# Kernel tuning notes

Measured on AMD Instinct MI355X. Metric: run time of the kernel, lower is better.

## Reference

```python
import jax, jax.numpy as jnp
import numpy as np
from jax import lax

H = 64        # hidden_dim
M = 5         # num_modes
T_OUT = 6

def _gru_step(h, x, W_ih, W_hh, b_ih, b_hh):
    # torch GRU/GRUCell math; W_* are [3H, in] torch layout
    gi = x @ W_ih.T + b_ih
    gh = h @ W_hh.T + b_hh
    i_r, i_z, i_n = jnp.split(gi, 3, axis=-1)
    h_r, h_z, h_n = jnp.split(gh, 3, axis=-1)
    r = jax.nn.sigmoid(i_r + h_r)
    z = jax.nn.sigmoid(i_z + h_z)
    n = jnp.tanh(i_n + r * h_n)
    return (1.0 - z) * n + z * h

def _edges(B, N):
    # all ordered pairs i != j per sample (row-major like the python double loop),
    # then self loops for every node (PyG GATConv add_self_loops=True)
    s, d = np.nonzero(~np.eye(N, dtype=bool))
    off = (np.arange(B) * N)[:, None]
    src = (s[None, :] + off).ravel()
    dst = (d[None, :] + off).ravel()
    loops = np.arange(B * N)
    return np.concatenate([src, loops]), np.concatenate([dst, loops]), src.shape[0]

def reference(x, embed_W, embed_b, gat_W, gat_att_src, gat_att_dst, gat_b,
              enc_Wih, enc_Whh, enc_bih, enc_bhh,
              dec_Wih, dec_Whh, dec_bih, dec_bhh,
              out_W1, out_b1, out_W2, out_b2, proj_W, proj_b,
              conf_W1, conf_b1, conf_W2, conf_b2):
    B, T, N, _ = x.shape
    BN = B * N
    x_emb = x @ embed_W + embed_b                      # (B,T,N,H)

    # --- GRU encoder over time, batched over B*N nodes ---
    seq = x_emb.transpose(1, 0, 2, 3).reshape(T, BN, H)
    def enc_step(h, xt):
        return _gru_step(h, xt, enc_Wih, enc_Whh, enc_bih, enc_bhh), None
    h_enc, _ = lax.scan(enc_step, jnp.zeros((BN, H), x.dtype), seq)  # (BN,H)

    # --- GATConv (1 head, eval mode => no dropout) on last-frame embeddings ---
    mask = (x[:, -1, :, 0:6].sum(-1) != 0).reshape(BN)
    src_np, dst_np, n_pair = _edges(B, N)
    src = jnp.asarray(src_np); dst = jnp.asarray(dst_np)
    valid = jnp.concatenate([mask[src[:n_pair]] & mask[dst[:n_pair]],
                             jnp.ones((BN,), bool)])  # self loops always present
    xl = x_emb[:, -1].reshape(BN, H) @ gat_W           # (BN,H) transformed feats
    a_s = xl @ gat_att_src                             # (BN,)
    a_d = xl @ gat_att_dst
    alpha = jax.nn.leaky_relu(a_s[src] + a_d[dst], 0.2)
    amax = jax.ops.segment_max(jnp.where(valid, alpha, -1e30), dst, num_segments=BN)
    e = jnp.where(valid, jnp.exp(alpha - amax[dst]), 0.0)
    denom = jax.ops.segment_sum(e, dst, num_segments=BN)
    w = e / denom[dst]
    gat_out = jax.ops.segment_sum(w[:, None] * xl[src], dst, num_segments=BN) + gat_b

    h_final = h_enc + gat_out                          # (BN,H)

    # --- GRUCell decoder loop ---
    dec_in = (x[:, -1, :, 0:2] @ proj_W + proj_b).reshape(BN, H)
    def dec_step(carry, _):
        h, di = carry
        h = _gru_step(h, di, dec_Wih, dec_Whh, dec_bih, dec_bhh)
        o = jax.nn.relu(h @ out_W1 + out_b1) @ out_W2 + out_b2   # (BN, 2M)
        o = o.reshape(B, N, 2, M)
        nxt = (o[..., 0] @ proj_W + proj_b).reshape(BN, H)       # mode-0 xy fed back
        return (h, nxt), o
    _, outs = lax.scan(dec_step, (h_final, dec_in), None, length=T_OUT)  # (T_OUT,B,N,2,M)
    traj = outs.transpose(1, 4, 2, 0, 3)               # (B, M, N, T_OUT, 2)

    hf = h_final.reshape(B, N, H)
    conf = jax.nn.softmax(jax.nn.relu(hf @ conf_W1 + conf_b1) @ conf_W2 + conf_b2, axis=-1)
    return traj, conf.transpose(0, 2, 1)               # (B, M, N)

def setup_inputs() -> dict:
    key = jax.random.key(0)
    ks = jax.random.split(key, 25)
    n = lambda k, s: jax.random.normal(k, s, jnp.float32) * 0.1
    B, T, N, Fd = 32768, 5, 5, 10
    return {
        "x": jax.random.normal(ks[0], (B, T, N, Fd), jnp.float32),
        "embed_W": n(ks[1], (Fd, H)), "embed_b": n(ks[2], (H,)),
        "gat_W": n(ks[3], (H, H)), "gat_att_src": n(ks[4], (H,)),
        "gat_att_dst": n(ks[5], (H,)), "gat_b": n(ks[6], (H,)),
        "enc_Wih": n(ks[7], (3 * H, H)), "enc_Whh": n(ks[8], (3 * H, H)),
        "enc_bih": n(ks[9], (3 * H,)), "enc_bhh": n(ks[10], (3 * H,)),
        "dec_Wih": n(ks[11], (3 * H, H)), "dec_Whh": n(ks[12], (3 * H, H)),
        "dec_bih": n(ks[13], (3 * H,)), "dec_bhh": n(ks[14], (3 * H,)),
        "out_W1": n(ks[15], (H, 64)), "out_b1": n(ks[16], (64,)),
        "out_W2": n(ks[17], (64, 2 * M)), "out_b2": n(ks[18], (2 * M,)),
        "proj_W": n(ks[19], (2, H)), "proj_b": n(ks[20], (H,)),
        "conf_W1": n(ks[21], (H, 64)), "conf_b1": n(ks[22], (64,)),
        "conf_W2": n(ks[23], (64, M)), "conf_b2": n(ks[24], (M,)),
    }
```

## Files before the change

### kernel.cpp

```cpp
#include <hip/hip_runtime.h>

#define HDIM 64
#define NMODE 5
#define TOUT 6
#define TIN 5
#define NNODE 5
#define FD 10

typedef short bf16x8 __attribute__((ext_vector_type(8)));
typedef float f32x4 __attribute__((ext_vector_type(4)));

#define MFMA16(A,B,C) __builtin_amdgcn_mfma_f32_16x16x32_bf16((A),(B),(C),0,0,0)


__device__ __forceinline__ float fastrcp(float x){ return __builtin_amdgcn_rcpf(x); }
__device__ __forceinline__ float sigm(float x){ return fastrcp(1.f + __expf(-x)); }
__device__ __forceinline__ float tanh_f(float x){ return 2.f*fastrcp(1.f + __expf(-2.f*x)) - 1.f; }

__device__ __forceinline__ short f2b(float f){
  unsigned u = __float_as_uint(f);
  unsigned r = (u + 0x7FFFu + ((u >> 16) & 1u)) >> 16;
  return (short)r;
}
__device__ __forceinline__ float b2f(short s){
  return __uint_as_float(((unsigned)(unsigned short)s) << 16);
}
__device__ __forceinline__ int hswz(int row, int col){
  return row*64 + ((((col>>3) ^ (row&7)))<<3) + (col&7);
}

__global__ void setup_kernel(
    const float* __restrict__ embed_W, const float* __restrict__ embed_b,
    const float* __restrict__ enc_Wih, const float* __restrict__ enc_bih,
    const float* __restrict__ enc_Whh, const float* __restrict__ enc_bhh,
    const float* __restrict__ dec_Wih, const float* __restrict__ dec_bih,
    const float* __restrict__ dec_Whh, const float* __restrict__ dec_bhh,
    const float* __restrict__ proj_W,  const float* __restrict__ proj_b,
    const float* __restrict__ gat_W,   const float* __restrict__ gat_as,
    const float* __restrict__ gat_ad,  const float* __restrict__ gat_b,
    const float* __restrict__ out_W1,  const float* __restrict__ out_W2,
    const float* __restrict__ conf_W1, const float* __restrict__ conf_W2,
    short* __restrict__ wsb)
{
  float* wsf  = (float*)(wsb) + 26880;
  float* WcET = wsf;        float* WcDT = wsf+1920;
  float* bcE  = wsf+2304;   float* bcD  = wsf+2496;
  float* brzE = wsf+2688;   float* brzD = wsf+2816;
  float* EG   = wsf+2944;   float* ebg0 = wsf+3584;
  float* egs  = wsf+3648;   float* egd  = wsf+3658;
  float* c6   = wsf+3668;
  const int t = threadIdx.x;

  for (int i = t; i < 1920; i += 256){ int n=i/10, f=i%10; float s=0.f;
    for(int e=0;e<64;e++) s += embed_W[f*64+e]*enc_Wih[n*64+e]; WcET[i]=s; }
  for (int i = t; i < 384; i += 256){ int n=i/2, c=i%2; float s=0.f;
    for(int e=0;e<64;e++) s += proj_W[c*64+e]*dec_Wih[n*64+e]; WcDT[i]=s; }
  for (int n = t; n < 192; n += 256){
    float s=enc_bih[n]; for(int e=0;e<64;e++) s += embed_b[e]*enc_Wih[n*64+e]; bcE[n]=s;
    float d=dec_bih[n]; for(int e=0;e<64;e++) d += proj_b[e]*dec_Wih[n*64+e]; bcD[n]=d; }
  for (int i = t; i < 640; i += 256){ int f=i/64, n=i%64; float s=0.f;
    for(int e=0;e<64;e++) s += embed_W[f*64+e]*gat_W[e*64+n]; EG[i]=s; }
  for (int n = t; n < 64; n += 256){ float s=0.f;
    for(int e=0;e<64;e++) s += embed_b[e]*gat_W[e*64+n]; ebg0[n]=s; }
  __syncthreads();
  for (int n = t; n < 128; n += 256){ brzE[n]=bcE[n]+enc_bhh[n]; brzD[n]=bcD[n]+dec_bhh[n]; }
  for (int f = t; f < 10; f += 256){ float s=0.f, d=0.f;
    for(int n=0;n<64;n++){ s += EG[f*64+n]*gat_as[n]; d += EG[f*64+n]*gat_ad[n]; }
    egs[f]=s; egd[f]=d; }
  if (t == 0){ float s=0.f, d=0.f;
    for(int n=0;n<64;n++){ s += ebg0[n]*gat_as[n]; d += ebg0[n]*gat_ad[n]; }
    c6[0]=s; c6[1]=d; }
  __syncthreads();

  for (int i = t; i < 18432; i += 256){
    int nt=i/1536, r=i%1536, kt=r>>9, r2=r&511, lane=r2>>3, j=r2&7;
    int k=kt*32+(lane>>4)*8+j, n=nt*16+(lane&15);
    float v=0.f;
    if (k < 64) v = enc_Whh[n*64+k];
    else if (k < 74){ if (n < 128) v = WcET[n*10+(k-64)]; }
    else if (k == 74) v = (n < 128) ? brzE[n] : enc_bhh[n];
    wsb[i]=f2b(v);
  }
  for (int i = t; i < 2048; i += 256){
    int nt=i>>9, r2=i&511, lane=r2>>3, j=r2&7;
    int k=64+(lane>>4)*8+j, n=128+nt*16+(lane&15);
    float v=0.f;
    if (k < 74) v = WcET[n*10+(k-64)];
    else if (k == 74) v = bcE[n];
    wsb[18432+i]=f2b(v);
  }
  for (int i = t; i < 18432; i += 256){
    int nt=i/1536, r=i%1536, kt=r>>9, r2=r&511, lane=r2>>3, j=r2&7;
    int k=kt*32+(lane>>4)*8+j, n=nt*16+(lane&15);
    float v=0.f;
    if (k < 64) v = dec_Whh[n*64+k];
    else if (k < 66){ if (n < 128) v = WcDT[n*2+(k-64)]; }
    else if (k == 66) v = (n < 128) ? brzD[n] : dec_bhh[n];
    wsb[20480+i]=f2b(v);
  }
  for (int i = t; i < 2048; i += 256){
    int nt=i>>9, r2=i&511, lane=r2>>3, j=r2&7;
    int k=64+(lane>>4)*8+j, n=128+nt*16+(lane&15);
    float v=0.f;
    if (k < 66) v = WcDT[n*2+(k-64)];
    else if (k == 66) v = bcD[n];
    wsb[38912+i]=f2b(v);
  }
  for (int i = t; i < 2560; i += 256){
    int nt=i>>9, r2=i&511, lane=r2>>3, j=r2&7;
    int k=64+(lane>>4)*8+j, n=nt*16+(lane&15);
    float v=0.f;
    if (k < 74){ int f=k-64;
      if (n < 64) v = EG[f*64+n]; else if (n == 64) v = egs[f]; else if (n == 65) v = egd[f];
    } else if (k == 74){
      if (n < 64) v = ebg0[n]+gat_b[n]; else if (n == 64) v = c6[0]; else if (n == 65) v = c6[1];
    }
    wsb[40960+i]=f2b(v);
  }
  for (int i = t; i < 4096; i += 256){
    int nt=i>>10, r=i&1023, kt=r>>9, r2=r&511, lane=r2>>3, j=r2&7;
    int k=kt*32+(lane>>4)*8+j, n=nt*16+(lane&15);
    wsb[43520+i]=f2b(out_W1 [k*64+n]);
    wsb[48640+i]=f2b(conf_W1[k*64+n]);
  }
  for (int i = t; i < 1024; i += 256){
    int kt=i>>9, r2=i&511, lane=r2>>3, j=r2&7;
    int k=kt*32+(lane>>4)*8+j, n=lane&15;
    wsb[47616+i]=f2b(n<10 ? out_W2 [k*10+n] : 0.f);
    wsb[52736+i]=f2b(n<5  ? conf_W2[k*5 +n] : 0.f);
  }
}

__device__ __forceinline__ void gru_mfma_step(const short* Bs, short* hS,
    float (&hcd)[4][4], bf16x8 af2, int wid, int lane)
{
  const int g = lane>>4, l15 = lane&15;
  const int arow = wid*16 + l15;
  const int sw = arow & 7;
  bf16x8 af0 = *(const bf16x8*)&hS[arow*64 + (((0+g) ^ sw)<<3)];
  bf16x8 af1 = *(const bf16x8*)&hS[arow*64 + (((4+g) ^ sw)<<3)];
  f32x4 acc[12];
  #pragma unroll
  for (int nt = 0; nt < 12; nt++){
    f32x4 a = {0.f,0.f,0.f,0.f};
    a = MFMA16(af0, *(const bf16x8*)&Bs[(nt*3+0)*512 + lane*8], a);
    a = MFMA16(af1, *(const bf16x8*)&Bs[(nt*3+1)*512 + lane*8], a);
    a = MFMA16(af2, *(const bf16x8*)&Bs[(nt*3+2)*512 + lane*8], a);
    acc[nt] = a;
  }
  f32x4 accx[4];
  #pragma unroll
  for (int nt = 0; nt < 4; nt++){
    f32x4 a = {0.f,0.f,0.f,0.f};
    accx[nt] = MFMA16(af2, *(const bf16x8*)&Bs[18432 + nt*512 + lane*8], a);
  }
  #pragma unroll
  for (int nt = 0; nt < 4; nt++){
    #pragma unroll
    for (int j = 0; j < 4; j++){
      float r  = sigm(acc[nt][j]);
      float z  = sigm(acc[nt+4][j]);
      float ng = tanh_f(accx[nt][j] + r*acc[nt+8][j]);
      float hn = (1.f - z)*ng + z*hcd[nt][j];
      hcd[nt][j] = hn;
      hS[hswz(wid*16 + 4*g + j, nt*16 + l15)] = f2b(hn);
    }
  }
}

__global__ __launch_bounds__(256, 2) void model_kernel(
    const float* __restrict__ x, const short* __restrict__ wsb,
    const float* __restrict__ out_b1, const float* __restrict__ out_b2,
    const float* __restrict__ conf_b1, const float* __restrict__ conf_b2,
    float* __restrict__ traj, float* __restrict__ conf, int B)
{
  __shared__ __align__(16) short Bs[20480];
  __shared__ __align__(16) short hS[4096];
  __shared__ __align__(16) short sS[4096];
  __shared__ float xyS[128];
  __shared__ float asdS[128];
  __shared__ float maskS[64];

  const int tid = threadIdx.x;
  const int wid = tid>>6, lane = tid&63;
  const int g = lane>>4, l15 = lane&15;
  const int BN = B*NNODE;
  const int br0 = blockIdx.x*60;
  const int arow = wid*16 + l15;
  const short ONE = 0x3F80;

  float b1r[4], cb1r[4];
  #pragma unroll
  for (int nt = 0; nt < 4; nt++){ b1r[nt]=out_b1[nt*16+l15]; cb1r[nt]=conf_b1[nt*16+l15]; }
  const float b2r  = out_b2 [l15<10 ? l15 : 0];
  const float cb2r = conf_b2[l15<5  ? l15 : 0];

  int growA = br0 + arow; if (growA > BN-1) growA = BN-1;
  const float* xrow = x + (size_t)(growA/5)*250 + (growA%5)*10;

  for (int i = tid; i < 2560; i += 256) ((int4*)Bs)[i] = ((const int4*)wsb)[i];
  for (int i = tid; i < 4096; i += 256) hS[i] = 0;
  float hcd[4][4];
  #pragma unroll
  for (int a1=0;a1<4;a1++){
    #pragma unroll
    for (int a2=0;a2<4;a2++) hcd[a1][a2]=0.f;
  }
  __syncthreads();

  for (int t = 0; t < TIN; t++){
    bf16x8 af2 = {0,0,0,0,0,0,0,0};
    if (g == 0){
      const float2* p = (const float2*)(xrow + t*50);
      float2 v0=p[0], v1=p[1], v2=p[2], v3=p[3];
      af2[0]=f2b(v0.x); af2[1]=f2b(v0.y); af2[2]=f2b(v1.x); af2[3]=f2b(v1.y);
      af2[4]=f2b(v2.x); af2[5]=f2b(v2.y); af2[6]=f2b(v3.x); af2[7]=f2b(v3.y);
    } else if (g == 1){
      const float2* p = (const float2*)(xrow + t*50 + 8);
      float2 v4=p[0];
      af2[0]=f2b(v4.x); af2[1]=f2b(v4.y); af2[2]=ONE;
    }
    gru_mfma_step(Bs, hS, hcd, af2, wid, lane);
    __syncthreads();
  }

  {
    bf16x8 af2 = {0,0,0,0,0,0,0,0};
    if (g == 0){
      const float2* p = (const float2*)(xrow + 4*50);
      float2 v0=p[0], v1=p[1], v2=p[2], v3=p[3];
      af2[0]=f2b(v0.x); af2[1]=f2b(v0.y); af2[2]=f2b(v1.x); af2[3]=f2b(v1.y);
      af2[4]=f2b(v2.x); af2[5]=f2b(v2.y); af2[6]=f2b(v3.x); af2[7]=f2b(v3.y);
      float msum = v0.x+v0.y+v1.x+v1.y+v2.x+v2.y;
      maskS[arow] = (msum != 0.f) ? 1.f : 0.f;
      xyS[arow*2]   = v0.x;
      xyS[arow*2+1] = v0.y;
    } else if (g == 1){
      const float2* p = (const float2*)(xrow + 4*50 + 8);
      float2 v4=p[0];
      af2[0]=f2b(v4.x); af2[1]=f2b(v4.y); af2[2]=ONE;
    }
    #pragma unroll
    for (int nt = 0; nt < 5; nt++){
      f32x4 a = {0.f,0.f,0.f,0.f};
      a = MFMA16(af2, *(const bf16x8*)(wsb + 40960 + nt*512 + lane*8), a);
      if (nt < 4){
        #pragma unroll
        for (int j = 0; j < 4; j++)
          sS[(wid*16 + 4*g + j)*64 + nt*16 + l15] = f2b(a[j]);
      } else if (l15 < 2){
        #pragma unroll
        for (int j = 0; j < 4; j++)
          asdS[(wid*16 + 4*g + j)*2 + l15] = a[j];
      }
    }
  }
  __syncthreads();
  {
    int dst = tid >> 2, cb = tid & 3;
    if (dst < 60){
      int nd = dst % 5, bas = dst - nd;
      float ad  = asdS[dst*2+1];
      float mkD = maskS[dst];
      float al[5], mx = -1e30f;
      #pragma unroll
      for (int i = 0; i < 5; i++){
        float a = asdS[(bas+i)*2] + ad;
        a = (a > 0.f) ? a : 0.2f*a;
        bool valid = (i == nd) || (maskS[bas+i] != 0.f && mkD != 0.f);
        al[i] = valid ? a : -1e30f;
        mx = fmaxf(mx, al[i]);
      }
      float w5[5], es = 0.f;
      #pragma unroll
      for (int i = 0; i < 5; i++){ float e = (al[i] > -1e29f) ? __expf(al[i]-mx) : 0.f; w5[i]=e; es+=e; }
      float rs = fastrcp(es);
      #pragma unroll
      for (int i = 0; i < 5; i++) w5[i] *= rs;
      for (int cc = 0; cc < 16; cc++){
        int c = cb*16 + cc;
        float agg = 0.f;
        #pragma unroll
        for (int i = 0; i < 5; i++) agg += w5[i]*b2f(sS[(bas+i)*64 + c]);
        int hi = hswz(dst, c);
        hS[hi] = f2b(b2f(hS[hi]) + agg);
      }
    }
  }
  __syncthreads();
  #pragma unroll
  for (int nt = 0; nt < 4; nt++){
    #pragma unroll
    for (int j = 0; j < 4; j++)
      hcd[nt][j] = b2f(hS[hswz(wid*16+4*g+j, nt*16+l15)]);
  }

  {
    const int sw = arow & 7;
    bf16x8 hf0 = *(const bf16x8*)&hS[arow*64 + (((0+g) ^ sw)<<3)];
    bf16x8 hf1 = *(const bf16x8*)&hS[arow*64 + (((4+g) ^ sw)<<3)];
    #pragma unroll
    for (int nt = 0; nt < 4; nt++){
      f32x4 a = {0.f,0.f,0.f,0.f};
      a = MFMA16(hf0, *(const bf16x8*)(wsb + 48640 + (nt*2+0)*512 + lane*8), a);
      a = MFMA16(hf1, *(const bf16x8*)(wsb + 48640 + (nt*2+1)*512 + lane*8), a);
      #pragma unroll
      for (int j = 0; j < 4; j++)
        sS[hswz(wid*16+4*g+j, nt*16+l15)] = f2b(fmaxf(a[j] + cb1r[nt], 0.f));
    }
    __syncthreads();
    bf16x8 sf0 = *(const bf16x8*)&sS[arow*64 + (((0+g) ^ sw)<<3)];
    bf16x8 sf1 = *(const bf16x8*)&sS[arow*64 + (((4+g) ^ sw)<<3)];
    f32x4 a = {0.f,0.f,0.f,0.f};
    a = MFMA16(sf0, *(const bf16x8*)(wsb + 52736 + 0*512 + lane*8), a);
    a = MFMA16(sf1, *(const bf16x8*)(wsb + 52736 + 1*512 + lane*8), a);
    #pragma unroll
    for (int j = 0; j < 4; j++){
      float my = a[j] + cb2r;
      float v0 = __shfl(my, (lane&48)+0, 64);
      float v1 = __shfl(my, (lane&48)+1, 64);
      float v2 = __shfl(my, (lane&48)+2, 64);
      float v3 = __shfl(my, (lane&48)+3, 64);
      float v4 = __shfl(my, (lane&48)+4, 64);
      float mx = fmaxf(fmaxf(fmaxf(v0,v1),fmaxf(v2,v3)),v4);
      float es = __expf(v0-mx)+__expf(v1-mx)+__expf(v2-mx)+__expf(v3-mx)+__expf(v4-mx);
      int lrow = wid*16 + 4*g + j;
      int gr = br0 + lrow;
      if (l15 < 5 && lrow < 60 && gr < BN){
        int samp = gr/5, node = gr - samp*5;
        conf[((size_t)samp*NMODE + l15)*NNODE + node] = __expf(my-mx)*fastrcp(es);
      }
    }
    __syncthreads();
  }

  for (int i = tid; i < 2560; i += 256) ((int4*)Bs)[i] = ((const int4*)(wsb + 20480))[i];
  __syncthreads();

  for (int t = 0; t < TOUT; t++){
    bf16x8 af2 = {0,0,0,0,0,0,0,0};
    if (g == 0){
      af2[0] = f2b(xyS[arow*2]);
      af2[1] = f2b(xyS[arow*2+1]);
      af2[2] = ONE;
    }
    gru_mfma_step(Bs, hS, hcd, af2, wid, lane);
    __syncthreads();

    const int sw = arow & 7;
    bf16x8 hf0 = *(const bf16x8*)&hS[arow*64 + (((0+g) ^ sw)<<3)];
    bf16x8 hf1 = *(const bf16x8*)&hS[arow*64 + (((4+g) ^ sw)<<3)];
    #pragma unroll
    for (int nt = 0; nt < 4; nt++){
      f32x4 a = {0.f,0.f,0.f,0.f};
      a = MFMA16(hf0, *(const bf16x8*)(wsb + 43520 + (nt*2+0)*512 + lane*8), a);
      a = MFMA16(hf1, *(const bf16x8*)(wsb + 43520 + (nt*2+1)*512 + lane*8), a);
      #pragma unroll
      for (int j = 0; j < 4; j++)
        sS[hswz(wid*16+4*g+j, nt*16+l15)] = f2b(fmaxf(a[j] + b1r[nt], 0.f));
    }
    __syncthreads();
    bf16x8 sf0 = *(const bf16x8*)&sS[arow*64 + (((0+g) ^ sw)<<3)];
    bf16x8 sf1 = *(const bf16x8*)&sS[arow*64 + (((4+g) ^ sw)<<3)];
    f32x4 oo = {0.f,0.f,0.f,0.f};
    oo = MFMA16(sf0, *(const bf16x8*)(wsb + 47616 + 0*512 + lane*8), oo);
    oo = MFMA16(sf1, *(const bf16x8*)(wsb + 47616 + 1*512 + lane*8), oo);
    #pragma unroll
    for (int j = 0; j < 4; j++){
      float ov = oo[j] + b2r;
      int lrow = wid*16 + 4*g + j;
      int gr = br0 + lrow;
      if (l15 < 10 && lrow < 60 && gr < BN){
        int samp = gr/5, node = gr - samp*5;
        int cc = (l15 >= 5) ? 1 : 0;
        int m = l15 - 5*cc;
        traj[((size_t)(samp*NMODE + m)*NNODE + node)*(TOUT*2) + t*2 + cc] = ov;
      }
      if (l15 == 0) xyS[lrow*2]   = ov;
      if (l15 == 5) xyS[lrow*2+1] = ov;
    }
    __syncthreads();
  }
}

extern "C" void kernel_launch(void* const* d_in, const int* in_sizes, int n_in,
                              void* d_out, int out_size, void* d_ws, size_t ws_size,
                              hipStream_t stream)
{
  const float* x           = (const float*)d_in[0];
  const float* embed_W     = (const float*)d_in[1];
  const float* embed_b     = (const float*)d_in[2];
  const float* gat_W       = (const float*)d_in[3];
  const float* gat_att_src = (const float*)d_in[4];
  const float* gat_att_dst = (const float*)d_in[5];
  const float* gat_b       = (const float*)d_in[6];
  const float* enc_Wih     = (const float*)d_in[7];
  const float* enc_Whh     = (const float*)d_in[8];
  const float* enc_bih     = (const float*)d_in[9];
  const float* enc_bhh     = (const float*)d_in[10];
  const float* dec_Wih     = (const float*)d_in[11];
  const float* dec_Whh     = (const float*)d_in[12];
  const float* dec_bih     = (const float*)d_in[13];
  const float* dec_bhh     = (const float*)d_in[14];
  const float* out_W1      = (const float*)d_in[15];
  const float* out_b1      = (const float*)d_in[16];
  const float* out_W2      = (const float*)d_in[17];
  const float* out_b2      = (const float*)d_in[18];
  const float* proj_W      = (const float*)d_in[19];
  const float* proj_b      = (const float*)d_in[20];
  const float* conf_W1     = (const float*)d_in[21];
  const float* conf_b1     = (const float*)d_in[22];
  const float* conf_W2     = (const float*)d_in[23];
  const float* conf_b2     = (const float*)d_in[24];

  const int B = in_sizes[0] / (TIN*NNODE*FD);
  const int BN = B*NNODE;
  short* wsb = (short*)d_ws;
  float* traj = (float*)d_out;
  float* conf = traj + (size_t)B*NMODE*NNODE*TOUT*2;

  setup_kernel<<<1, 256, 0, stream>>>(embed_W, embed_b, enc_Wih, enc_bih, enc_Whh, enc_bhh,
                                      dec_Wih, dec_bih, dec_Whh, dec_bhh, proj_W, proj_b,
                                      gat_W, gat_att_src, gat_att_dst, gat_b,
                                      out_W1, out_W2, conf_W1, conf_W2, wsb);

  const int blocks = (BN + 59)/60;
  model_kernel<<<blocks, 256, 0, stream>>>(x, wsb, out_b1, out_b2, conf_b1, conf_b2,
                                           traj, conf, B);
}
```

Baseline: 396.3 us.

## Shrink LDS weights, replace block syncs with wave barriers, parallelize setup

The single-block setup kernel is split into a 4-block fold kernel and a 64-block fragment-packing kernel, so the serial preprocessing runs in parallel. In the GRU step only the hidden-weight K tiles stay in LDS. The rarely-nonzero input/bias tile and the extra n-gate tiles are now read from global memory, which cuts LDS per block and lets launch bounds target 3 blocks per CU. Because each wave only touches its own 16 rows of hS and sS, the block-wide __syncthreads are replaced by wave barriers. This risks extra global/L2 traffic for the MFMA B operands and relies on per-wave ownership being strict.

```diff
diff --git a/kernel.cpp b/kernel.cpp
--- a/kernel.cpp
+++ b/kernel.cpp
@@ -29,17 +29,14 @@
   return row*64 + ((((col>>3) ^ (row&7)))<<3) + (col&7);
 }
 
-__global__ void setup_kernel(
+__global__ void setup_fold(
     const float* __restrict__ embed_W, const float* __restrict__ embed_b,
     const float* __restrict__ enc_Wih, const float* __restrict__ enc_bih,
-    const float* __restrict__ enc_Whh, const float* __restrict__ enc_bhh,
     const float* __restrict__ dec_Wih, const float* __restrict__ dec_bih,
-    const float* __restrict__ dec_Whh, const float* __restrict__ dec_bhh,
     const float* __restrict__ proj_W,  const float* __restrict__ proj_b,
     const float* __restrict__ gat_W,   const float* __restrict__ gat_as,
-    const float* __restrict__ gat_ad,  const float* __restrict__ gat_b,
-    const float* __restrict__ out_W1,  const float* __restrict__ out_W2,
-    const float* __restrict__ conf_W1, const float* __restrict__ conf_W2,
+    const float* __restrict__ gat_ad,
+    const float* __restrict__ enc_bhh, const float* __restrict__ dec_bhh,
     short* __restrict__ wsb)
 {
   float* wsf  = (float*)(wsb) + 26880;
@@ -49,30 +46,56 @@
   float* EG   = wsf+2944;   float* ebg0 = wsf+3584;
   float* egs  = wsf+3648;   float* egd  = wsf+3658;
   float* c6   = wsf+3668;
-  const int t = threadIdx.x;
-
-  for (int i = t; i < 1920; i += 256){ int n=i/10, f=i%10; float s=0.f;
-    for(int e=0;e<64;e++) s += embed_W[f*64+e]*enc_Wih[n*64+e]; WcET[i]=s; }
-  for (int i = t; i < 384; i += 256){ int n=i/2, c=i%2; float s=0.f;
-    for(int e=0;e<64;e++) s += proj_W[c*64+e]*dec_Wih[n*64+e]; WcDT[i]=s; }
-  for (int n = t; n < 192; n += 256){
-    float s=enc_bih[n]; for(int e=0;e<64;e++) s += embed_b[e]*enc_Wih[n*64+e]; bcE[n]=s;
-    float d=dec_bih[n]; for(int e=0;e<64;e++) d += proj_b[e]*dec_Wih[n*64+e]; bcD[n]=d; }
-  for (int i = t; i < 640; i += 256){ int f=i/64, n=i%64; float s=0.f;
-    for(int e=0;e<64;e++) s += embed_W[f*64+e]*gat_W[e*64+n]; EG[i]=s; }
-  for (int n = t; n < 64; n += 256){ float s=0.f;
-    for(int e=0;e<64;e++) s += embed_b[e]*gat_W[e*64+n]; ebg0[n]=s; }
-  __syncthreads();
-  for (int n = t; n < 128; n += 256){ brzE[n]=bcE[n]+enc_bhh[n]; brzD[n]=bcD[n]+dec_bhh[n]; }
-  for (int f = t; f < 10; f += 256){ float s=0.f, d=0.f;
-    for(int n=0;n<64;n++){ s += EG[f*64+n]*gat_as[n]; d += EG[f*64+n]*gat_ad[n]; }
-    egs[f]=s; egd[f]=d; }
-  if (t == 0){ float s=0.f, d=0.f;
-    for(int n=0;n<64;n++){ s += ebg0[n]*gat_as[n]; d += ebg0[n]*gat_ad[n]; }
-    c6[0]=s; c6[1]=d; }
-  __syncthreads();
-
-  for (int i = t; i < 18432; i += 256){
+  const int t = threadIdx.x, bx = blockIdx.x;
+
+  if (bx <= 1){
+    for (int i = bx*960 + t; i < (bx+1)*960; i += 256){
+      int n=i/10, f=i%10; float s=0.f;
+      for(int e=0;e<64;e++) s += embed_W[f*64+e]*enc_Wih[n*64+e];
+      WcET[i]=s;
+    }
+  } else if (bx == 2){
+    for (int i = t; i < 384; i += 256){ int n=i/2, c=i%2; float s=0.f;
+      for(int e=0;e<64;e++) s += proj_W[c*64+e]*dec_Wih[n*64+e]; WcDT[i]=s; }
+    for (int n = t; n < 192; n += 256){
+      float s=enc_bih[n]; for(int e=0;e<64;e++) s += embed_b[e]*enc_Wih[n*64+e]; bcE[n]=s;
+      float d=dec_bih[n]; for(int e=0;e<64;e++) d += proj_b[e]*dec_Wih[n*64+e]; bcD[n]=d; }
+    __syncthreads();
+    for (int n = t; n < 128; n += 256){ brzE[n]=bcE[n]+enc_bhh[n]; brzD[n]=bcD[n]+dec_bhh[n]; }
+  } else if (bx == 3){
+    for (int i = t; i < 640; i += 256){ int f=i/64, n=i%64; float s=0.f;
+      for(int e=0;e<64;e++) s += embed_W[f*64+e]*gat_W[e*64+n]; EG[i]=s; }
+    for (int n = t; n < 64; n += 256){ float s=0.f;
+      for(int e=0;e<64;e++) s += embed_b[e]*gat_W[e*64+n]; ebg0[n]=s; }
+    __syncthreads();
+    for (int f = t; f < 10; f += 256){ float s=0.f, d=0.f;
+      for(int n=0;n<64;n++){ s += EG[f*64+n]*gat_as[n]; d += EG[f*64+n]*gat_ad[n]; }
+      egs[f]=s; egd[f]=d; }
+    if (t == 0){ float s=0.f, d=0.f;
+      for(int n=0;n<64;n++){ s += ebg0[n]*gat_as[n]; d += ebg0[n]*gat_ad[n]; }
+      c6[0]=s; c6[1]=d; }
+  }
+}
+
+__global__ void setup_frag(
+    const float* __restrict__ enc_Whh, const float* __restrict__ enc_bhh,
+    const float* __restrict__ dec_Whh, const float* __restrict__ dec_bhh,
+    const float* __restrict__ gat_b,
+    const float* __restrict__ out_W1,  const float* __restrict__ out_W2,
+    const float* __restrict__ conf_W1, const float* __restrict__ conf_W2,
+    short* __restrict__ wsb)
+{
+  const float* wsf  = (const float*)(wsb) + 26880;
+  const float* WcET = wsf;        const float* WcDT = wsf+1920;
+  const float* bcE  = wsf+2304;   const float* bcD  = wsf+2496;
+  const float* brzE = wsf+2688;   const float* brzD = wsf+2816;
+  const float* EG   = wsf+2944;   const float* ebg0 = wsf+3584;
+  const float* egs  = wsf+3648;   const float* egd  = wsf+3658;
+  const float* c6   = wsf+3668;
+  const int gt = blockIdx.x*256 + threadIdx.x;
+  const int gs = gridDim.x*256;
+
+  for (int i = gt; i < 18432; i += gs){
     int nt=i/1536, r=i%1536, kt=r>>9, r2=r&511, lane=r2>>3, j=r2&7;
     int k=kt*32+(lane>>4)*8+j, n=nt*16+(lane&15);
     float v=0.f;
@@ -81,7 +104,7 @@
     else if (k == 74) v = (n < 128) ? brzE[n] : enc_bhh[n];
     wsb[i]=f2b(v);
   }
-  for (int i = t; i < 2048; i += 256){
+  for (int i = gt; i < 2048; i += gs){
     int nt=i>>9, r2=i&511, lane=r2>>3, j=r2&7;
     int k=64+(lane>>4)*8+j, n=128+nt*16+(lane&15);
     float v=0.f;
@@ -89,7 +112,7 @@
     else if (k == 74) v = bcE[n];
     wsb[18432+i]=f2b(v);
   }
-  for (int i = t; i < 18432; i += 256){
+  for (int i = gt; i < 18432; i += gs){
     int nt=i/1536, r=i%1536, kt=r>>9, r2=r&511, lane=r2>>3, j=r2&7;
     int k=kt*32+(lane>>4)*8+j, n=nt*16+(lane&15);
     float v=0.f;
@@ -98,7 +121,7 @@
     else if (k == 66) v = (n < 128) ? brzD[n] : dec_bhh[n];
     wsb[20480+i]=f2b(v);
   }
-  for (int i = t; i < 2048; i += 256){
+  for (int i = gt; i < 2048; i += gs){
     int nt=i>>9, r2=i&511, lane=r2>>3, j=r2&7;
     int k=64+(lane>>4)*8+j, n=128+nt*16+(lane&15);
     float v=0.f;
@@ -106,7 +129,7 @@
     else if (k == 66) v = bcD[n];
     wsb[38912+i]=f2b(v);
   }
-  for (int i = t; i < 2560; i += 256){
+  for (int i = gt; i < 2560; i += gs){
     int nt=i>>9, r2=i&511, lane=r2>>3, j=r2&7;
     int k=64+(lane>>4)*8+j, n=nt*16+(lane&15);
     float v=0.f;
@@ -117,13 +140,13 @@
     }
     wsb[40960+i]=f2b(v);
   }
-  for (int i = t; i < 4096; i += 256){
+  for (int i = gt; i < 4096; i += gs){
     int nt=i>>10, r=i&1023, kt=r>>9, r2=r&511, lane=r2>>3, j=r2&7;
     int k=kt*32+(lane>>4)*8+j, n=nt*16+(lane&15);
     wsb[43520+i]=f2b(out_W1 [k*64+n]);
     wsb[48640+i]=f2b(conf_W1[k*64+n]);
   }
-  for (int i = t; i < 1024; i += 256){
+  for (int i = gt; i < 1024; i += gs){
     int kt=i>>9, r2=i&511, lane=r2>>3, j=r2&7;
     int k=kt*32+(lane>>4)*8+j, n=lane&15;
     wsb[47616+i]=f2b(n<10 ? out_W2 [k*10+n] : 0.f);
@@ -131,8 +154,8 @@
   }
 }
 
-__device__ __forceinline__ void gru_mfma_step(const short* Bs, short* hS,
-    float (&hcd)[4][4], bf16x8 af2, int wid, int lane)
+__device__ __forceinline__ void gru_mfma_step(const short* BsL, const short* __restrict__ Bg,
+    short* hS, float (&hcd)[4][4], bf16x8 af2, int wid, int lane)
 {
   const int g = lane>>4, l15 = lane&15;
   const int arow = wid*16 + l15;
@@ -143,16 +166,16 @@
   #pragma unroll
   for (int nt = 0; nt < 12; nt++){
     f32x4 a = {0.f,0.f,0.f,0.f};
-    a = MFMA16(af0, *(const bf16x8*)&Bs[(nt*3+0)*512 + lane*8], a);
-    a = MFMA16(af1, *(const bf16x8*)&Bs[(nt*3+1)*512 + lane*8], a);
-    a = MFMA16(af2, *(const bf16x8*)&Bs[(nt*3+2)*512 + lane*8], a);
+    a = MFMA16(af0, *(const bf16x8*)&BsL[(nt*2+0)*512 + lane*8], a);
+    a = MFMA16(af1, *(const bf16x8*)&BsL[(nt*2+1)*512 + lane*8], a);
+    a = MFMA16(af2, *(const bf16x8*)&Bg[(nt*3+2)*512 + lane*8], a);
     acc[nt] = a;
   }
   f32x4 accx[4];
   #pragma unroll
   for (int nt = 0; nt < 4; nt++){
     f32x4 a = {0.f,0.f,0.f,0.f};
-    accx[nt] = MFMA16(af2, *(const bf16x8*)&Bs[18432 + nt*512 + lane*8], a);
+    accx[nt] = MFMA16(af2, *(const bf16x8*)&Bg[18432 + nt*512 + lane*8], a);
   }
   #pragma unroll
   for (int nt = 0; nt < 4; nt++){
@@ -166,15 +189,16 @@
       hS[hswz(wid*16 + 4*g + j, nt*16 + l15)] = f2b(hn);
     }
   }
-}
-
-__global__ __launch_bounds__(256, 2) void model_kernel(
+  __builtin_amdgcn_wave_barrier();
+}
+
+__global__ __launch_bounds__(256, 3) void model_kernel(
     const float* __restrict__ x, const short* __restrict__ wsb,
     const float* __restrict__ out_b1, const float* __restrict__ out_b2,
     const float* __restrict__ conf_b1, const float* __restrict__ conf_b2,
     float* __restrict__ traj, float* __restrict__ conf, int B)
 {
-  __shared__ __align__(16) short Bs[20480];
+  __shared__ __align__(16) short Bs[12288];
   __shared__ __align__(16) short hS[4096];
   __shared__ __align__(16) short sS[4096];
   __shared__ float xyS[128];
@@ -198,7 +222,10 @@
   int growA = br0 + arow; if (growA > BN-1) growA = BN-1;
   const float* xrow = x + (size_t)(growA/5)*250 + (growA%5)*10;
 
-  for (int i = tid; i < 2560; i += 256) ((int4*)Bs)[i] = ((const int4*)wsb)[i];
+  for (int i = tid; i < 1536; i += 256){
+    int f = i>>6, e = i&63, nt = f>>1, kt = f&1;
+    ((int4*)Bs)[f*64 + e] = ((const int4*)wsb)[(nt*3+kt)*64 + e];
+  }
   for (int i = tid; i < 4096; i += 256) hS[i] = 0;
   float hcd[4][4];
   #pragma unroll
@@ -220,8 +247,7 @@
       float2 v4=p[0];
       af2[0]=f2b(v4.x); af2[1]=f2b(v4.y); af2[2]=ONE;
     }
-    gru_mfma_step(Bs, hS, hcd, af2, wid, lane);
-    __syncthreads();
+    gru_mfma_step(Bs, wsb, hS, hcd, af2, wid, lane);
   }
 
   {
@@ -308,7 +334,7 @@
       for (int j = 0; j < 4; j++)
         sS[hswz(wid*16+4*g+j, nt*16+l15)] = f2b(fmaxf(a[j] + cb1r[nt], 0.f));
     }
-    __syncthreads();
+    __builtin_amdgcn_wave_barrier();
     bf16x8 sf0 = *(const bf16x8*)&sS[arow*64 + (((0+g) ^ sw)<<3)];
     bf16x8 sf1 = *(const bf16x8*)&sS[arow*64 + (((4+g) ^ sw)<<3)];
     f32x4 a = {0.f,0.f,0.f,0.f};
@@ -331,12 +357,15 @@
         conf[((size_t)samp*NMODE + l15)*NNODE + node] = __expf(my-mx)*fastrcp(es);
       }
     }
-    __syncthreads();
-  }
-
-  for (int i = tid; i < 2560; i += 256) ((int4*)Bs)[i] = ((const int4*)(wsb + 20480))[i];
+  }
+
+  for (int i = tid; i < 1536; i += 256){
+    int f = i>>6, e = i&63, nt = f>>1, kt = f&1;
+    ((int4*)Bs)[f*64 + e] = ((const int4*)(wsb + 20480))[(nt*3+kt)*64 + e];
+  }
   __syncthreads();
 
+  const short* Bgd = wsb + 20480;
   for (int t = 0; t < TOUT; t++){
     bf16x8 af2 = {0,0,0,0,0,0,0,0};
     if (g == 0){
@@ -344,8 +373,7 @@
       af2[1] = f2b(xyS[arow*2+1]);
       af2[2] = ONE;
     }
-    gru_mfma_step(Bs, hS, hcd, af2, wid, lane);
-    __syncthreads();
+    gru_mfma_step(Bs, Bgd, hS, hcd, af2, wid, lane);
 
     const int sw = arow & 7;
     bf16x8 hf0 = *(const bf16x8*)&hS[arow*64 + (((0+g) ^ sw)<<3)];
@@ -359,7 +387,7 @@
       for (int j = 0; j < 4; j++)
         sS[hswz(wid*16+4*g+j, nt*16+l15)] = f2b(fmaxf(a[j] + b1r[nt], 0.f));
     }
-    __syncthreads();
+    __builtin_amdgcn_wave_barrier();
     bf16x8 sf0 = *(const bf16x8*)&sS[arow*64 + (((0+g) ^ sw)<<3)];
     bf16x8 sf1 = *(const bf16x8*)&sS[arow*64 + (((4+g) ^ sw)<<3)];
     f32x4 oo = {0.f,0.f,0.f,0.f};
@@ -379,7 +407,7 @@
       if (l15 == 0) xyS[lrow*2]   = ov;
       if (l15 == 5) xyS[lrow*2+1] = ov;
     }
-    __syncthreads();
+    __builtin_amdgcn_wave_barrier();
   }
 }
 
@@ -419,10 +447,12 @@
   float* traj = (float*)d_out;
   float* conf = traj + (size_t)B*NMODE*NNODE*TOUT*2;
 
-  setup_kernel<<<1, 256, 0, stream>>>(embed_W, embed_b, enc_Wih, enc_bih, enc_Whh, enc_bhh,
-                                      dec_Wih, dec_bih, dec_Whh, dec_bhh, proj_W, proj_b,
-                                      gat_W, gat_att_src, gat_att_dst, gat_b,
-                                      out_W1, out_W2, conf_W1, conf_W2, wsb);
+  setup_fold<<<4, 256, 0, stream>>>(embed_W, embed_b, enc_Wih, enc_bih,
+                                    dec_Wih, dec_bih, proj_W, proj_b,
+                                    gat_W, gat_att_src, gat_att_dst,
+                                    enc_bhh, dec_bhh, wsb);
+  setup_frag<<<64, 256, 0, stream>>>(enc_Whh, enc_bhh, dec_Whh, dec_bhh, gat_b,
+                                     out_W1, out_W2, conf_W1, conf_W2, wsb);
 
   const int blocks = (BN + 59)/60;
   model_kernel<<<blocks, 256, 0, stream>>>(x, wsb, out_b1, out_b2, conf_b1, conf_b2,
```

Result: slower. 701.7 us (+77.1%).
